# Kernel tuning notes

Measured on AMD Instinct MI355X. Metric: run time of the kernel, lower is better.

## Reference

```python
import jax, jax.numpy as jnp
import numpy as np

H = W = 256
C = 256
N_ROIS = 2000
POOL = 7


def setup_inputs() -> dict:
    key = jax.random.key(0)
    kf, kw, kh, kx, ky = jax.random.split(key, 5)
    feature_map = jax.random.normal(kf, (1, H, W, C), dtype=jnp.float32)
    # ROI format: (batch_idx, x, y, w, h), integer pixel coords, in-bounds
    w = jax.random.randint(kw, (N_ROIS,), 8, 65)
    h = jax.random.randint(kh, (N_ROIS,), 8, 65)
    x = jax.random.randint(kx, (N_ROIS,), 0, W - 64)
    y = jax.random.randint(ky, (N_ROIS,), 0, H - 64)
    rois = jnp.stack([jnp.zeros_like(x), x, y, w, h], axis=1).astype(jnp.int32)
    return {"feature_map": feature_map, "rois": rois, "pool_size": POOL}


def _axis_coords(start, length, pool_size):
    """Sample coords along one axis, matching tf.image.resize bilinear
    (half-pixel centers) applied to the crop [start, start+length).
    start, length: [N] int. Returns abs idx0, idx1 [N,P] int and frac [N,P]."""
    lf = length.astype(jnp.float32)
    # source coord within the crop for each output pixel
    f = (jnp.arange(pool_size, dtype=jnp.float32) + 0.5)[None, :] * (lf / pool_size)[:, None] - 0.5
    f = jnp.clip(f, 0.0, (lf - 1.0)[:, None])
    i0 = jnp.floor(f).astype(jnp.int32)
    i1 = jnp.minimum(i0 + 1, (length - 1)[:, None])
    frac = f - i0.astype(jnp.float32)
    return start[:, None] + i0, start[:, None] + i1, frac


def _roi_pool(feature_map, rois, pool_size):
    fm = feature_map[0]                      # [H, W, C]
    x, y, w, h = rois[:, 1], rois[:, 2], rois[:, 3], rois[:, 4]
    y0, y1, fy = _axis_coords(y, h, pool_size)   # [N, P]
    x0, x1, fx = _axis_coords(x, w, pool_size)   # [N, P]

    def g(yi, xi):  # gather -> [N, P, P, C]
        return fm[yi[:, :, None], xi[:, None, :], :]

    fx_ = fx[:, None, :, None]
    fy_ = fy[:, :, None, None]
    top = g(y0, x0) * (1.0 - fx_) + g(y0, x1) * fx_
    bot = g(y1, x0) * (1.0 - fx_) + g(y1, x1) * fx_
    return top * (1.0 - fy_) + bot * fy_     # [N, P, P, C]


def reference(feature_map, rois, pool_size):
    return _roi_pool(feature_map, rois, pool_size)
```

## Files before the change

kernel.cpp:

```cpp
#include <hip/hip_runtime.h>

#define FH 256
#define FW 256
#define FC 256
#define POOL 7

typedef float f32x4 __attribute__((ext_vector_type(4)));

__global__ __launch_bounds__(256) void roi_pool_kernel(
    const float* __restrict__ fm,
    const int*   __restrict__ rois,
    float*       __restrict__ out,
    int n_rois)
{
    int nwg  = gridDim.x;
    int q    = nwg >> 3;
    int rr   = nwg & 7;
    int xcd  = blockIdx.x & 7;
    int slot = blockIdx.x >> 3;
    int base = (xcd < rr) ? xcd * (q + 1) : rr * (q + 1) + (xcd - rr) * q;
    int lb   = base + slot;

    int t = lb * 256 + (int)threadIdx.x;
    int total = n_rois * POOL * POOL * (FC / 4);
    if (t >= total) return;

    int lane = t & 63;
    int cell = t >> 6;
    int pi   = cell % POOL;
    int tmp  = cell / POOL;
    int pj   = tmp % POOL;
    int roi  = tmp / POOL;

    int rx = rois[roi * 5 + 1];
    int ry = rois[roi * 5 + 2];
    int rw = rois[roi * 5 + 3];
    int rh = rois[roi * 5 + 4];

    float lfh = (float)rh;
    float fy  = ((float)pj + 0.5f) * (lfh / (float)POOL) - 0.5f;
    fy = fminf(fmaxf(fy, 0.0f), lfh - 1.0f);
    int   j0 = (int)floorf(fy);
    int   j1 = min(j0 + 1, rh - 1);
    float wy = fy - (float)j0;
    int   y0 = ry + j0;
    int   y1 = ry + j1;

    float lfw = (float)rw;
    float fx  = ((float)pi + 0.5f) * (lfw / (float)POOL) - 0.5f;
    fx = fminf(fmaxf(fx, 0.0f), lfw - 1.0f);
    int   i0 = (int)floorf(fx);
    int   i1 = min(i0 + 1, rw - 1);
    float wx = fx - (float)i0;
    int   x0 = rx + i0;
    int   x1 = rx + i1;

    const f32x4* p00 = (const f32x4*)(fm + ((size_t)y0 * FW + x0) * FC) + lane;
    const f32x4* p01 = (const f32x4*)(fm + ((size_t)y0 * FW + x1) * FC) + lane;
    const f32x4* p10 = (const f32x4*)(fm + ((size_t)y1 * FW + x0) * FC) + lane;
    const f32x4* p11 = (const f32x4*)(fm + ((size_t)y1 * FW + x1) * FC) + lane;

    f32x4 a = *p00;
    f32x4 b = *p01;
    f32x4 c = *p10;
    f32x4 d = *p11;

    float owx = 1.0f - wx;
    float owy = 1.0f - wy;

    f32x4 top = a * owx + b * wx;
    f32x4 bot = c * owx + d * wx;
    f32x4 res = top * owy + bot * wy;

    f32x4* o = (f32x4*)(out + (size_t)cell * FC) + lane;
    __builtin_nontemporal_store(res, o);
}

extern "C" void kernel_launch(void* const* d_in, const int* in_sizes, int n_in,
                              void* d_out, int out_size, void* d_ws, size_t ws_size,
                              hipStream_t stream) {
    const float* fm   = (const float*)d_in[0];
    const int*   rois = (const int*)d_in[1];
    float* out = (float*)d_out;

    int n_rois = in_sizes[1] / 5;
    int total  = n_rois * POOL * POOL * (FC / 4);
    int block  = 256;
    int grid   = (total + block - 1) / block;

    roi_pool_kernel<<<grid, block, 0, stream>>>(fm, rois, out, n_rois);
}
```

Baseline: 182.3 us.

## Sort pooling cells by feature-map tile before gathering to improve locality

Adds a counting-sort pipeline (zero, histogram, scan, scatter) that buckets the output cells by the 16x16 spatial tile of their top-left sample. The main kernel then processes cells in tile order, so concurrently running wavefronts touch nearby feature-map rows and get more cache reuse. The cost is four extra small kernel launches and atomic contention, plus an indirect load per wavefront. A direct fallback kernel is kept for when workspace is missing.

```diff
diff --git a/kernel.cpp b/kernel.cpp
--- a/kernel.cpp
+++ b/kernel.cpp
@@ -5,13 +5,84 @@
 #define FC 256
 #define POOL 7
 
+#define TILE_SHIFT 4
+#define TILES_X (FW >> TILE_SHIFT)
+#define NTILES (TILES_X * (FH >> TILE_SHIFT))
+
 typedef float f32x4 __attribute__((ext_vector_type(4)));
+
+__device__ __forceinline__ int cell_tile(const int* __restrict__ rois, int cell)
+{
+    int pi  = cell % POOL;
+    int tmp = cell / POOL;
+    int pj  = tmp % POOL;
+    int roi = tmp / POOL;
+    int rx = rois[roi * 5 + 1];
+    int ry = rois[roi * 5 + 2];
+    int rw = rois[roi * 5 + 3];
+    int rh = rois[roi * 5 + 4];
+
+    float fy = ((float)pj + 0.5f) * ((float)rh / (float)POOL) - 0.5f;
+    fy = fminf(fmaxf(fy, 0.0f), (float)rh - 1.0f);
+    int y0 = ry + (int)floorf(fy);
+
+    float fx = ((float)pi + 0.5f) * ((float)rw / (float)POOL) - 0.5f;
+    fx = fminf(fmaxf(fx, 0.0f), (float)rw - 1.0f);
+    int x0 = rx + (int)floorf(fx);
+
+    return (y0 >> TILE_SHIFT) * TILES_X + (x0 >> TILE_SHIFT);
+}
+
+__global__ void zero_kernel(int* __restrict__ hist)
+{
+    hist[threadIdx.x] = 0;
+}
+
+__global__ __launch_bounds__(256) void hist_kernel(
+    const int* __restrict__ rois, int* __restrict__ hist, int n_cells)
+{
+    __shared__ int lh[NTILES];
+    int tid = threadIdx.x;
+    lh[tid] = 0;
+    __syncthreads();
+    int c = blockIdx.x * blockDim.x + tid;
+    if (c < n_cells) atomicAdd(&lh[cell_tile(rois, c)], 1);
+    __syncthreads();
+    int v = lh[tid];
+    if (v) atomicAdd(&hist[tid], v);
+}
+
+__global__ void scan_kernel(const int* __restrict__ hist, int* __restrict__ cursor)
+{
+    __shared__ int tmp[NTILES];
+    int i = threadIdx.x;
+    tmp[i] = hist[i];
+    __syncthreads();
+    if (i == 0) {
+        int acc = 0;
+        for (int k = 0; k < NTILES; ++k) { int v = tmp[k]; tmp[k] = acc; acc += v; }
+    }
+    __syncthreads();
+    cursor[i] = tmp[i];
+}
+
+__global__ __launch_bounds__(256) void scatter_kernel(
+    const int* __restrict__ rois, int* __restrict__ cursor,
+    int* __restrict__ sorted, int n_cells)
+{
+    int c = blockIdx.x * blockDim.x + threadIdx.x;
+    if (c >= n_cells) return;
+    int t = cell_tile(rois, c);
+    int pos = atomicAdd(&cursor[t], 1);
+    sorted[pos] = c;
+}
 
 __global__ __launch_bounds__(256) void roi_pool_kernel(
     const float* __restrict__ fm,
     const int*   __restrict__ rois,
+    const int*   __restrict__ sorted,
     float*       __restrict__ out,
-    int n_rois)
+    int n_cells)
 {
     int nwg  = gridDim.x;
     int q    = nwg >> 3;
@@ -21,12 +92,11 @@
     int base = (xcd < rr) ? xcd * (q + 1) : rr * (q + 1) + (xcd - rr) * q;
     int lb   = base + slot;
 
-    int t = lb * 256 + (int)threadIdx.x;
-    int total = n_rois * POOL * POOL * (FC / 4);
-    if (t >= total) return;
-
-    int lane = t & 63;
-    int cell = t >> 6;
+    int widx = lb * 4 + ((int)threadIdx.x >> 6);
+    if (widx >= n_cells) return;
+    int lane = threadIdx.x & 63;
+
+    int cell = sorted[widx];
     int pi   = cell % POOL;
     int tmp  = cell / POOL;
     int pj   = tmp % POOL;
@@ -76,6 +146,67 @@
     __builtin_nontemporal_store(res, o);
 }
 
+__global__ __launch_bounds__(256) void roi_pool_direct(
+    const float* __restrict__ fm,
+    const int*   __restrict__ rois,
+    float*       __restrict__ out,
+    int n_rois)
+{
+    int t = blockIdx.x * blockDim.x + (int)threadIdx.x;
+    int total = n_rois * POOL * POOL * (FC / 4);
+    if (t >= total) return;
+
+    int lane = t & 63;
+    int cell = t >> 6;
+    int pi   = cell % POOL;
+    int tmp  = cell / POOL;
+    int pj   = tmp % POOL;
+    int roi  = tmp / POOL;
+
+    int rx = rois[roi * 5 + 1];
+    int ry = rois[roi * 5 + 2];
+    int rw = rois[roi * 5 + 3];
+    int rh = rois[roi * 5 + 4];
+
+    float lfh = (float)rh;
+    float fy  = ((float)pj + 0.5f) * (lfh / (float)POOL) - 0.5f;
+    fy = fminf(fmaxf(fy, 0.0f), lfh - 1.0f);
+    int   j0 = (int)floorf(fy);
+    int   j1 = min(j0 + 1, rh - 1);
+    float wy = fy - (float)j0;
+    int   y0 = ry + j0;
+    int   y1 = ry + j1;
+
+    float lfw = (float)rw;
+    float fx  = ((float)pi + 0.5f) * (lfw / (float)POOL) - 0.5f;
+    fx = fminf(fmaxf(fx, 0.0f), lfw - 1.0f);
+    int   i0 = (int)floorf(fx);
+    int   i1 = min(i0 + 1, rw - 1);
+    float wx = fx - (float)i0;
+    int   x0 = rx + i0;
+    int   x1 = rx + i1;
+
+    const f32x4* p00 = (const f32x4*)(fm + ((size_t)y0 * FW + x0) * FC) + lane;
+    const f32x4* p01 = (const f32x4*)(fm + ((size_t)y0 * FW + x1) * FC) + lane;
+    const f32x4* p10 = (const f32x4*)(fm + ((size_t)y1 * FW + x0) * FC) + lane;
+    const f32x4* p11 = (const f32x4*)(fm + ((size_t)y1 * FW + x1) * FC) + lane;
+
+    f32x4 a = *p00;
+    f32x4 b = *p01;
+    f32x4 c = *p10;
+    f32x4 d = *p11;
+
+    float owx = 1.0f - wx;
+    float owy = 1.0f - wy;
+
+    f32x4 top = a * owx + b * wx;
+    f32x4 bot = c * owx + d * wx;
+    f32x4 res = top * owy + bot * wy;
+
+    f32x4* o = (f32x4*)(out + (size_t)cell * FC) + lane;
+    __builtin_nontemporal_store(res, o);
+}
+
 extern "C" void kernel_launch(void* const* d_in, const int* in_sizes, int n_in,
                               void* d_out, int out_size, void* d_ws, size_t ws_size,
                               hipStream_t stream) {
@@ -83,10 +214,29 @@
     const int*   rois = (const int*)d_in[1];
     float* out = (float*)d_out;
 
-    int n_rois = in_sizes[1] / 5;
-    int total  = n_rois * POOL * POOL * (FC / 4);
-    int block  = 256;
-    int grid   = (total + block - 1) / block;
-
-    roi_pool_kernel<<<grid, block, 0, stream>>>(fm, rois, out, n_rois);
-}
+    int n_rois  = in_sizes[1] / 5;
+    int n_cells = n_rois * POOL * POOL;
+
+    size_t ws_need = (size_t)(NTILES * 2 + n_cells) * sizeof(int);
+    if (ws_size < ws_need || d_ws == nullptr) {
+        int total = n_cells * (FC / 4);
+        int block = 256;
+        int grid  = (total + block - 1) / block;
+        roi_pool_direct<<<grid, block, 0, stream>>>(fm, rois, out, n_rois);
+        return;
+    }
+
+    int* hist   = (int*)d_ws;
+    int* cursor = hist + NTILES;
+    int* sorted = cursor + NTILES;
+
+    int bin_blocks = (n_cells + 255) / 256;
+
+    zero_kernel<<<1, NTILES, 0, stream>>>(hist);
+    hist_kernel<<<bin_blocks, 256, 0, stream>>>(rois, hist, n_cells);
+    scan_kernel<<<1, NTILES, 0, stream>>>(hist, cursor);
+    scatter_kernel<<<bin_blocks, 256, 0, stream>>>(rois, cursor, sorted, n_cells);
+
+    int pool_blocks = (n_cells + 3) / 4;
+    roi_pool_kernel<<<pool_blocks, 256, 0, stream>>>(fm, rois, sorted, out, n_cells);
+}
```

After: 286.4 us. 1.57x slower.

## Bin ROI sample cells by spatial tile so each block reuses local feature data

Applied to the files above, without the earlier changes.

Each block now owns a 16x16 spatial tile of the feature map plus one of 32 ROI subsets. It scans its ROIs in batches and uses a shared-memory queue to collect the sample cells whose top-left corner falls inside its tile, then interpolates them. The aim is for each block's gathers to hit a compact region so they reuse cache lines in L2/MALL. In exchange, every block rescans all ROIs in its subset, the per-block work is uneven, and the grid is 8192 blocks with many idle ones.

```diff
diff --git a/kernel.cpp b/kernel.cpp
--- a/kernel.cpp
+++ b/kernel.cpp
@@ -5,75 +5,133 @@
 #define FC 256
 #define POOL 7
 
+#define TILE_SHIFT 4
+#define TILES_X (FW >> TILE_SHIFT)
+#define TILES_Y (FH >> TILE_SHIFT)
+#define NTILES (TILES_X * TILES_Y)
+
+#define SUBS 32
+#define RBATCH 64
+#define QCAP (RBATCH * POOL * POOL)
+
 typedef float f32x4 __attribute__((ext_vector_type(4)));
 
-__global__ __launch_bounds__(256) void roi_pool_kernel(
+__global__ __launch_bounds__(256) void roi_pool_tiled(
     const float* __restrict__ fm,
     const int*   __restrict__ rois,
     float*       __restrict__ out,
     int n_rois)
 {
+    __shared__ int q[QCAP];
+    __shared__ int qn;
+
     int nwg  = gridDim.x;
-    int q    = nwg >> 3;
+    int qd   = nwg >> 3;
     int rr   = nwg & 7;
     int xcd  = blockIdx.x & 7;
     int slot = blockIdx.x >> 3;
-    int base = (xcd < rr) ? xcd * (q + 1) : rr * (q + 1) + (xcd - rr) * q;
+    int base = (xcd < rr) ? xcd * (qd + 1) : rr * (qd + 1) + (xcd - rr) * qd;
     int lb   = base + slot;
 
-    int t = lb * 256 + (int)threadIdx.x;
-    int total = n_rois * POOL * POOL * (FC / 4);
-    if (t >= total) return;
+    int tile = lb / SUBS;
+    int sub  = lb % SUBS;
+    int tly  = tile / TILES_X;
+    int tlx  = tile % TILES_X;
 
-    int lane = t & 63;
-    int cell = t >> 6;
-    int pi   = cell % POOL;
-    int tmp  = cell / POOL;
-    int pj   = tmp % POOL;
-    int roi  = tmp / POOL;
+    int tid  = threadIdx.x;
+    int lane = tid & 63;
+    int wav  = tid >> 6;
 
-    int rx = rois[roi * 5 + 1];
-    int ry = rois[roi * 5 + 2];
-    int rw = rois[roi * 5 + 3];
-    int rh = rois[roi * 5 + 4];
+    int nmine = (n_rois > sub) ? (n_rois - sub + SUBS - 1) / SUBS : 0;
+    int nbatch = (nmine + RBATCH - 1) / RBATCH;
 
-    float lfh = (float)rh;
-    float fy  = ((float)pj + 0.5f) * (lfh / (float)POOL) - 0.5f;
-    fy = fminf(fmaxf(fy, 0.0f), lfh - 1.0f);
-    int   j0 = (int)floorf(fy);
-    int   j1 = min(j0 + 1, rh - 1);
-    float wy = fy - (float)j0;
-    int   y0 = ry + j0;
-    int   y1 = ry + j1;
+    for (int b = 0; b < nbatch; ++b) {
+        if (tid == 0) qn = 0;
+        __syncthreads();
 
-    float lfw = (float)rw;
-    float fx  = ((float)pi + 0.5f) * (lfw / (float)POOL) - 0.5f;
-    fx = fminf(fmaxf(fx, 0.0f), lfw - 1.0f);
-    int   i0 = (int)floorf(fx);
-    int   i1 = min(i0 + 1, rw - 1);
-    float wx = fx - (float)i0;
-    int   x0 = rx + i0;
-    int   x1 = rx + i1;
+        int j = b * RBATCH + tid;
+        if (tid < RBATCH && j < nmine) {
+            int roi = sub + j * SUBS;
+            int rx = rois[roi * 5 + 1];
+            int ry = rois[roi * 5 + 2];
+            int rw = rois[roi * 5 + 3];
+            int rh = rois[roi * 5 + 4];
 
-    const f32x4* p00 = (const f32x4*)(fm + ((size_t)y0 * FW + x0) * FC) + lane;
-    const f32x4* p01 = (const f32x4*)(fm + ((size_t)y0 * FW + x1) * FC) + lane;
-    const f32x4* p10 = (const f32x4*)(fm + ((size_t)y1 * FW + x0) * FC) + lane;
-    const f32x4* p11 = (const f32x4*)(fm + ((size_t)y1 * FW + x1) * FC) + lane;
+            int ybits = 0, xbits = 0;
+            for (int p = 0; p < POOL; ++p) {
+                float fy = ((float)p + 0.5f) * ((float)rh / (float)POOL) - 0.5f;
+                fy = fminf(fmaxf(fy, 0.0f), (float)rh - 1.0f);
+                int y0 = ry + (int)floorf(fy);
+                if ((y0 >> TILE_SHIFT) == tly) ybits |= 1 << p;
 
-    f32x4 a = *p00;
-    f32x4 b = *p01;
-    f32x4 c = *p10;
-    f32x4 d = *p11;
+                float fx = ((float)p + 0.5f) * ((float)rw / (float)POOL) - 0.5f;
+                fx = fminf(fmaxf(fx, 0.0f), (float)rw - 1.0f);
+                int x0 = rx + (int)floorf(fx);
+                if ((x0 >> TILE_SHIFT) == tlx) xbits |= 1 << p;
+            }
+            if (ybits && xbits) {
+                int cnt = __popc(ybits) * __popc(xbits);
+                int p0  = atomicAdd(&qn, cnt);
+                for (int pj = 0; pj < POOL; ++pj) if (ybits & (1 << pj))
+                    for (int pi = 0; pi < POOL; ++pi) if (xbits & (1 << pi))
+                        q[p0++] = (roi * POOL + pj) * POOL + pi;
+            }
+        }
+        __syncthreads();
 
-    float owx = 1.0f - wx;
-    float owy = 1.0f - wy;
+        int n = qn;
+        for (int i = wav; i < n; i += 4) {
+            int cell = q[i];
+            int pi   = cell % POOL;
+            int tmp  = cell / POOL;
+            int pj   = tmp % POOL;
+            int roi  = tmp / POOL;
 
-    f32x4 top = a * owx + b * wx;
-    f32x4 bot = c * owx + d * wx;
-    f32x4 res = top * owy + bot * wy;
+            int rx = rois[roi * 5 + 1];
+            int ry = rois[roi * 5 + 2];
+            int rw = rois[roi * 5 + 3];
+            int rh = rois[roi * 5 + 4];
 
-    f32x4* o = (f32x4*)(out + (size_t)cell * FC) + lane;
-    __builtin_nontemporal_store(res, o);
+            float lfh = (float)rh;
+            float fy  = ((float)pj + 0.5f) * (lfh / (float)POOL) - 0.5f;
+            fy = fminf(fmaxf(fy, 0.0f), lfh - 1.0f);
+            int   j0 = (int)floorf(fy);
+            int   j1 = min(j0 + 1, rh - 1);
+            float wy = fy - (float)j0;
+            int   y0 = ry + j0;
+            int   y1 = ry + j1;
+
+            float lfw = (float)rw;
+            float fx  = ((float)pi + 0.5f) * (lfw / (float)POOL) - 0.5f;
+            fx = fminf(fmaxf(fx, 0.0f), lfw - 1.0f);
+            int   i0 = (int)floorf(fx);
+            int   i1 = min(i0 + 1, rw - 1);
+            float wx = fx - (float)i0;
+            int   x0 = rx + i0;
+            int   x1 = rx + i1;
+
+            const f32x4* p00 = (const f32x4*)(fm + ((size_t)y0 * FW + x0) * FC) + lane;
+            const f32x4* p01 = (const f32x4*)(fm + ((size_t)y0 * FW + x1) * FC) + lane;
+            const f32x4* p10 = (const f32x4*)(fm + ((size_t)y1 * FW + x0) * FC) + lane;
+            const f32x4* p11 = (const f32x4*)(fm + ((size_t)y1 * FW + x1) * FC) + lane;
+
+            f32x4 a = *p00;
+            f32x4 bb = *p01;
+            f32x4 c = *p10;
+            f32x4 d = *p11;
+
+            float owx = 1.0f - wx;
+            float owy = 1.0f - wy;
+
+            f32x4 top = a * owx + bb * wx;
+            f32x4 bot = c * owx + d * wx;
+            f32x4 res = top * owy + bot * wy;
+
+            f32x4* o = (f32x4*)(out + (size_t)cell * FC) + lane;
+            __builtin_nontemporal_store(res, o);
+        }
+        __syncthreads();
+    }
 }
 
 extern "C" void kernel_launch(void* const* d_in, const int* in_sizes, int n_in,
@@ -84,9 +142,7 @@
     float* out = (float*)d_out;
 
     int n_rois = in_sizes[1] / 5;
-    int total  = n_rois * POOL * POOL * (FC / 4);
-    int block  = 256;
-    int grid   = (total + block - 1) / block;
 
-    roi_pool_kernel<<<grid, block, 0, stream>>>(fm, rois, out, n_rois);
+    int grid = NTILES * SUBS;
+    roi_pool_tiled<<<grid, 256, 0, stream>>>(fm, rois, out, n_rois);
 }
```

Result: no change. 184.3 us (+1.1%).

## Stage feature-map tiles in LDS and bin ROI cells per spatial tile

Applied to the files above, without the earlier changes.

Each workgroup now owns a 16x16 spatial tile (with a one-pixel halo) of one 64-channel slice. It loads that slice into LDS once, then scans all ROIs in batches of 64. For each batch it builds an LDS queue of the output cells whose top-left sample falls in its tile and interpolates those cells from LDS. This replaces four scattered global gathers per output with one coalesced tile load. The cost is that every workgroup serially scans all ROIs, with several barriers and atomics per batch, and the large LDS footprint limits occupancy.

```diff
diff --git a/kernel.cpp b/kernel.cpp
--- a/kernel.cpp
+++ b/kernel.cpp
@@ -5,75 +5,133 @@
 #define FC 256
 #define POOL 7
 
+
+#define TS 16
+#define TP 17
+#define CQ 64
+#define NCQ (FC/CQ)
+#define TILES_X (FW/TS)
+#define NTILES (TILES_X*(FH/TS))
+#define RB 64
+#define QCAP (RB*POOL*POOL)
+
 typedef float f32x4 __attribute__((ext_vector_type(4)));
 
-__global__ __launch_bounds__(256) void roi_pool_kernel(
+__global__ __launch_bounds__(256) void roi_pool_lds(
     const float* __restrict__ fm,
     const int*   __restrict__ rois,
     float*       __restrict__ out,
     int n_rois)
 {
+    __shared__ float tilebuf[TP*TP*CQ];
+    __shared__ unsigned short q[QCAP];
+    __shared__ int lroi[RB];
+    __shared__ int qn;
+
     int nwg  = gridDim.x;
-    int q    = nwg >> 3;
+    int qd   = nwg >> 3;
     int rr   = nwg & 7;
     int xcd  = blockIdx.x & 7;
-    int slot = blockIdx.x >> 3;
-    int base = (xcd < rr) ? xcd * (q + 1) : rr * (q + 1) + (xcd - rr) * q;
-    int lb   = base + slot;
+    int slt  = blockIdx.x >> 3;
+    int base = (xcd < rr) ? xcd*(qd+1) : rr*(qd+1) + (xcd-rr)*qd;
+    int lb   = base + slt;
 
-    int t = lb * 256 + (int)threadIdx.x;
-    int total = n_rois * POOL * POOL * (FC / 4);
-    if (t >= total) return;
+    int cq      = lb & (NCQ-1);
+    int tile_id = lb >> 2;
+    int tly = tile_id / TILES_X;
+    int tlx = tile_id % TILES_X;
 
-    int lane = t & 63;
-    int cell = t >> 6;
-    int pi   = cell % POOL;
-    int tmp  = cell / POOL;
-    int pj   = tmp % POOL;
-    int roi  = tmp / POOL;
+    int tid  = threadIdx.x;
+    int lane = tid & 63;
+    int wav  = tid >> 6;
 
-    int rx = rois[roi * 5 + 1];
-    int ry = rois[roi * 5 + 2];
-    int rw = rois[roi * 5 + 3];
-    int rh = rois[roi * 5 + 4];
+    {
+        int s = tid & 15;
+        for (int p = tid >> 4; p < TP*TP; p += 16) {
+            int ly = p / TP, lx = p % TP;
+            int gy = min(tly*TS + ly, FH-1);
+            int gx = min(tlx*TS + lx, FW-1);
+            const f32x4* src = (const f32x4*)(fm + ((size_t)gy*FW + gx)*FC + cq*CQ) + s;
+            *(f32x4*)&tilebuf[p*CQ + s*4] = *src;
+        }
+    }
 
-    float lfh = (float)rh;
-    float fy  = ((float)pj + 0.5f) * (lfh / (float)POOL) - 0.5f;
-    fy = fminf(fmaxf(fy, 0.0f), lfh - 1.0f);
-    int   j0 = (int)floorf(fy);
-    int   j1 = min(j0 + 1, rh - 1);
-    float wy = fy - (float)j0;
-    int   y0 = ry + j0;
-    int   y1 = ry + j1;
+    int nb = (n_rois + RB - 1) / RB;
+    for (int b = 0; b < nb; ++b) {
+        __syncthreads();
+        if (tid == 0) qn = 0;
+        __syncthreads();
 
-    float lfw = (float)rw;
-    float fx  = ((float)pi + 0.5f) * (lfw / (float)POOL) - 0.5f;
-    fx = fminf(fmaxf(fx, 0.0f), lfw - 1.0f);
-    int   i0 = (int)floorf(fx);
-    int   i1 = min(i0 + 1, rw - 1);
-    float wx = fx - (float)i0;
-    int   x0 = rx + i0;
-    int   x1 = rx + i1;
+        if (tid < RB) {
+            int roi = b*RB + tid;
+            if (roi < n_rois) {
+                int rx = rois[roi*5+1];
+                int ry = rois[roi*5+2];
+                int rw = rois[roi*5+3];
+                int rh = rois[roi*5+4];
+                lroi[tid] = rx | (ry<<8) | (rw<<16) | (rh<<24);
+                int yb = 0, xb = 0;
+                for (int p = 0; p < POOL; ++p) {
+                    float fy = fminf(fmaxf(((float)p+0.5f)*((float)rh/(float)POOL)-0.5f, 0.f), (float)rh-1.f);
+                    int y0 = ry + (int)floorf(fy);
+                    if ((y0 >> 4) == tly) yb |= 1 << p;
+                    float fx = fminf(fmaxf(((float)p+0.5f)*((float)rw/(float)POOL)-0.5f, 0.f), (float)rw-1.f);
+                    int x0 = rx + (int)floorf(fx);
+                    if ((x0 >> 4) == tlx) xb |= 1 << p;
+                }
+                if (yb && xb) {
+                    int cnt = __popc(yb) * __popc(xb);
+                    int pos = atomicAdd(&qn, cnt);
+                    for (int pj = 0; pj < POOL; ++pj) if (yb & (1<<pj))
+                        for (int pi = 0; pi < POOL; ++pi) if (xb & (1<<pi))
+                            q[pos++] = (unsigned short)((tid<<6)|(pj<<3)|pi);
+                }
+            }
+        }
+        __syncthreads();
 
-    const f32x4* p00 = (const f32x4*)(fm + ((size_t)y0 * FW + x0) * FC) + lane;
-    const f32x4* p01 = (const f32x4*)(fm + ((size_t)y0 * FW + x1) * FC) + lane;
-    const f32x4* p10 = (const f32x4*)(fm + ((size_t)y1 * FW + x0) * FC) + lane;
-    const f32x4* p11 = (const f32x4*)(fm + ((size_t)y1 * FW + x1) * FC) + lane;
+        int n = qn;
+        for (int i = wav*4; i < n; i += 16) {
+            int e = i + (lane >> 4);
+            if (e < n) {
+                int pk = q[e];
+                int rl = pk >> 6;
+                int pj = (pk >> 3) & 7;
+                int pi = pk & 7;
+                int pr = lroi[rl];
+                int rx = pr & 255, ry = (pr>>8) & 255, rw = (pr>>16) & 255, rh = (pr>>24) & 255;
 
-    f32x4 a = *p00;
-    f32x4 b = *p01;
-    f32x4 c = *p10;
-    f32x4 d = *p11;
+                float fy = fminf(fmaxf(((float)pj+0.5f)*((float)rh/(float)POOL)-0.5f, 0.f), (float)rh-1.f);
+                int   j0 = (int)floorf(fy);
+                int   j1 = min(j0+1, rh-1);
+                float wy = fy - (float)j0;
+                float fx = fminf(fmaxf(((float)pi+0.5f)*((float)rw/(float)POOL)-0.5f, 0.f), (float)rw-1.f);
+                int   i0 = (int)floorf(fx);
+                int   i1 = min(i0+1, rw-1);
+                float wx = fx - (float)i0;
 
-    float owx = 1.0f - wx;
-    float owy = 1.0f - wy;
+                int ly0 = ry + j0 - tly*TS;
+                int ly1 = ry + j1 - tly*TS;
+                int lx0 = rx + i0 - tlx*TS;
+                int lx1 = rx + i1 - tlx*TS;
 
-    f32x4 top = a * owx + b * wx;
-    f32x4 bot = c * owx + d * wx;
-    f32x4 res = top * owy + bot * wy;
+                int s = lane & 15;
+                f32x4 a  = *(const f32x4*)&tilebuf[(ly0*TP+lx0)*CQ + s*4];
+                f32x4 bb = *(const f32x4*)&tilebuf[(ly0*TP+lx1)*CQ + s*4];
+                f32x4 c  = *(const f32x4*)&tilebuf[(ly1*TP+lx0)*CQ + s*4];
+                f32x4 d  = *(const f32x4*)&tilebuf[(ly1*TP+lx1)*CQ + s*4];
 
-    f32x4* o = (f32x4*)(out + (size_t)cell * FC) + lane;
-    __builtin_nontemporal_store(res, o);
+                float owx = 1.f - wx, owy = 1.f - wy;
+                f32x4 top = a*owx + bb*wx;
+                f32x4 bot = c*owx + d*wx;
+                f32x4 res = top*owy + bot*wy;
+
+                int roi  = b*RB + rl;
+                int cell = (roi*POOL + pj)*POOL + pi;
+                __builtin_nontemporal_store(res, (f32x4*)(out + (size_t)cell*FC + cq*CQ) + s);
+            }
+        }
+    }
 }
 
 extern "C" void kernel_launch(void* const* d_in, const int* in_sizes, int n_in,
@@ -82,11 +140,10 @@
     const float* fm   = (const float*)d_in[0];
     const int*   rois = (const int*)d_in[1];
     float* out = (float*)d_out;
+    (void)d_ws; (void)ws_size;
 
     int n_rois = in_sizes[1] / 5;
-    int total  = n_rois * POOL * POOL * (FC / 4);
-    int block  = 256;
-    int grid   = (total + block - 1) / block;
 
-    roi_pool_kernel<<<grid, block, 0, stream>>>(fm, rois, out, n_rois);
+    int grid = NTILES * NCQ;
+    roi_pool_lds<<<grid, 256, 0, stream>>>(fm, rois, out, n_rois);
 }
```

Result: slower. 284.8 us (+56.2%).
